# Kernel tuning notes

Hardware: AMD Instinct MI355X
Metric: run time of the kernel (lower is better)

Reference implementation:

```python
import jax, jax.numpy as jnp
import numpy as np

B, S, D = 2, 2048, 1024
N_QK, N_V, N_KNOW = 4096, 4096, 8192
N_HEADS = 16
MAX_K_QK, MAX_K_V, MAX_K_KNOW = 32, 32, 64
LN_EPS = 1e-6


def _unit_norm(key, shape, scale=1.0):
    x = jax.random.normal(key, shape, jnp.float32)
    return x / (jnp.linalg.norm(x, axis=-1, keepdims=True) + 1e-8) * scale


def setup_inputs() -> dict:
    key = jax.random.key(0)
    ks = jax.random.split(key, 12)
    return {
        "x": jax.random.normal(ks[0], (B, S, D), jnp.float32),
        "qk_emb": _unit_norm(ks[1], (N_QK, D)),
        "qk_w": _unit_norm(ks[2], (N_QK, D)),
        "v_emb": _unit_norm(ks[3], (N_V, D)),
        "v_w": _unit_norm(ks[4], (N_V, D)),
        "know_emb": _unit_norm(ks[5], (N_KNOW, D)),
        "know_w": _unit_norm(ks[6], (N_KNOW, D)),
        "tau_attn_k": jax.random.normal(ks[7], (D, 3), jnp.float32) * (1.0 / np.sqrt(D)),
        "tau_attn_b": jnp.zeros((3,), jnp.float32),
        "tau_know_k": jax.random.normal(ks[8], (D, 1), jnp.float32) * (1.0 / np.sqrt(D)),
        "tau_know_b": jnp.zeros((1,), jnp.float32),
        "expand_O": jax.random.normal(ks[9], (D, D), jnp.float32) * 0.02,
        "ln1_scale": jnp.ones((D,), jnp.float32),
        "ln1_bias": jnp.zeros((D,), jnp.float32),
        "ln2_scale": jnp.ones((D,), jnp.float32),
        "ln2_bias": jnp.zeros((D,), jnp.float32),
    }


def _layer_norm(x, scale, bias):
    mean = jnp.mean(x, axis=-1, keepdims=True)
    var = jnp.mean(jnp.square(x - mean), axis=-1, keepdims=True)
    return (x - mean) / jnp.sqrt(var + LN_EPS) * scale + bias


def threshold_gate(scores, tau, max_k):
    # scores: [B,S,N], tau: [B,S,1]
    raw = scores - tau
    gate = jnp.where(raw > 0, raw, 1e-8 * jnp.exp(raw))
    exp_gate = jnp.exp(gate) - 1.0
    topk_vals, _ = jax.lax.top_k(exp_gate, min(max_k, scores.shape[-1]))
    thr = topk_vals[:, :, -1:]
    exp_gate = jnp.where(exp_gate >= thr, exp_gate, 0.0)
    gate_sum = exp_gate.sum(axis=-1, keepdims=True) + 1e-8
    strength = jnp.tanh(exp_gate.max(axis=-1, keepdims=True))
    return exp_gate / gate_sum * strength


@jax.checkpoint
def sense_emit_full(x, emb, w, gate):
    # [B,S,D] @ [D,N] -> gated [B,S,N] -> [B,S,D]
    return ((x @ emb.T) * gate) @ w


def _block(x, qk_emb, qk_w, v_emb, v_w, know_emb, know_w,
           tau_attn_k, tau_attn_b, tau_know_k, tau_know_b,
           expand_O, ln1_scale, ln1_bias, ln2_scale, ln2_bias):
    # ---- attention circuit (deterministic; dropout = identity) ----
    normed = _layer_norm(x, ln1_scale, ln1_bias)
    scores_qk = normed @ qk_emb.T           # [B,S,N_QK]
    scores_v = normed @ v_emb.T             # [B,S,N_V]
    tau_all = normed @ tau_attn_k + tau_attn_b  # [B,S,3]
    g_Q = threshold_gate(scores_qk, tau_all[:, :, 0:1], MAX_K_QK)
    g_K = threshold_gate(scores_qk, tau_all[:, :, 1:2], MAX_K_QK)
    g_V = threshold_gate(scores_v, tau_all[:, :, 2:3], MAX_K_V)
    t_qk = 1.0 / qk_emb.shape[0]
    t_v = 1.0 / v_emb.shape[0]
    a_aux = (((g_Q.mean(axis=(0, 1)) - t_qk) ** 2).sum() * g_Q.shape[-1]
             + ((g_K.mean(axis=(0, 1)) - t_qk) ** 2).sum() * g_K.shape[-1]
             + ((g_V.mean(axis=(0, 1)) - t_v) ** 2).sum() * g_V.shape[-1])

    Q = sense_emit_full(normed, qk_emb, qk_w, g_Q)
    K = sense_emit_full(normed, qk_emb, qk_w, g_K)
    V = sense_emit_full(normed, v_emb, v_w, g_V)

    Bs, Ss, Ds = x.shape
    d_head = Ds // N_HEADS
    Q = Q.reshape(Bs, Ss, N_HEADS, d_head).transpose(0, 2, 1, 3)
    K = K.reshape(Bs, Ss, N_HEADS, d_head).transpose(0, 2, 1, 3)
    V = V.reshape(Bs, Ss, N_HEADS, d_head).transpose(0, 2, 1, 3)
    scale = jnp.sqrt(jnp.float32(d_head))
    attn = jnp.einsum('bhsd,bhtd->bhst', Q, K) / scale
    causal = jnp.tril(jnp.ones((Ss, Ss), dtype=jnp.bool_))
    attn = jnp.where(causal, attn, jnp.finfo(attn.dtype).min)
    attn = jax.nn.softmax(attn, axis=-1)
    out = jnp.einsum('bhst,bhtd->bhsd', attn, V)
    out = out.transpose(0, 2, 1, 3).reshape(Bs, Ss, Ds)
    out = out @ expand_O
    x = x + out

    # ---- knowledge circuit ----
    normed = _layer_norm(x, ln2_scale, ln2_bias)
    scores_k = normed @ know_emb.T          # [B,S,N_KNOW]
    tau_k = normed @ tau_know_k + tau_know_b
    gate = threshold_gate(scores_k, tau_k, MAX_K_KNOW)
    t_k = 1.0 / know_emb.shape[0]
    k_aux = ((gate.mean(axis=(0, 1)) - t_k) ** 2).sum() * know_emb.shape[0]
    know_out = sense_emit_full(normed, know_emb, know_w, gate)
    x = x + know_out
    return x, a_aux + k_aux


def reference(x, qk_emb, qk_w, v_emb, v_w, know_emb, know_w,
              tau_attn_k, tau_attn_b, tau_know_k, tau_know_b,
              expand_O, ln1_scale, ln1_bias, ln2_scale, ln2_bias):
    return _block(x, qk_emb, qk_w, v_emb, v_w, know_emb, know_w,
                  tau_attn_k, tau_attn_b, tau_know_k, tau_know_b,
                  expand_O, ln1_scale, ln1_bias, ln2_scale, ln2_bias)
```

## Files before the change

kernel.cpp:

```cpp
#include <hip/hip_runtime.h>

#define TOK   4096
#define DIM   1024
#define NQK   4096
#define NV    4096
#define NKN   8192
#define SLEN  2048
#define NH    16
#define DH    64
#define CAPA  48
#define CAPK  96
#define APAD  72

typedef float  f32x4  __attribute__((ext_vector_type(4)));
typedef short  short8 __attribute__((ext_vector_type(8)));
typedef unsigned int  u32;
typedef unsigned short u16;

__device__ __forceinline__ u16 f2bf(float f) {
    u32 u = __float_as_uint(f);
    u32 r = (u + 0x7fffu + ((u >> 16) & 1u)) >> 16;
    return (u16)r;
}
__device__ __forceinline__ float bf2f(u16 v) { return __uint_as_float(((u32)v) << 16); }

__device__ __forceinline__ f32x4 mfma_bf16(short8 a, short8 b, f32x4 c) {
    asm volatile("v_mfma_f32_16x16x32_bf16 %0, %1, %2, %0"
                 : "+v"(c) : "v"(a), "v"(b));
    return c;
}

__device__ __forceinline__ void gload16(const u16* g, u16* s) {
    __builtin_amdgcn_global_load_lds((const __attribute__((address_space(1))) void*)g,
                                     (__attribute__((address_space(3))) void*)s, 16, 0, 0);
}

__device__ __forceinline__ float blockReduceF(float v, float* red, int wave, int lane) {
#pragma unroll
    for (int off = 32; off > 0; off >>= 1) v += __shfl_xor(v, off);
    __syncthreads();
    if (lane == 0) red[wave] = v;
    __syncthreads();
    return red[0] + red[1] + red[2] + red[3];
}

__global__ __launch_bounds__(256) void k_f32_to_bf16(const float* __restrict__ in,
                                                     u16* __restrict__ out, int n4) {
    int i = blockIdx.x * 256 + threadIdx.x;
    int stride = gridDim.x * 256;
    for (; i < n4; i += stride) {
        float4 v = reinterpret_cast<const float4*>(in)[i];
        ushort4 o = make_ushort4(f2bf(v.x), f2bf(v.y), f2bf(v.z), f2bf(v.w));
        reinterpret_cast<ushort4*>(out)[i] = o;
    }
}

__global__ __launch_bounds__(256) void k_transpose_bf16(const float* __restrict__ in,
                                                        u16* __restrict__ out) {
    __shared__ float tile[32][33];
    int bx = blockIdx.x * 32;
    int by = blockIdx.y * 32;
    int tx = threadIdx.x & 31;
    int ty = threadIdx.x >> 5;
    for (int r = ty; r < 32; r += 8)
        tile[r][tx] = in[(size_t)(by + r) * DIM + bx + tx];
    __syncthreads();
    for (int r = ty; r < 32; r += 8)
        out[(size_t)(bx + r) * DIM + by + tx] = f2bf(tile[tx][r]);
}

__global__ __launch_bounds__(256) void k_ln_tau(const float* __restrict__ x,
                                                const float* __restrict__ sc,
                                                const float* __restrict__ bi,
                                                const float* __restrict__ tauk,
                                                const float* __restrict__ taub,
                                                int ntau,
                                                u16* __restrict__ nrm,
                                                float* __restrict__ tau_out) {
    __shared__ float red[4];
    int t = blockIdx.x, tid = threadIdx.x, wave = tid >> 6, lane = tid & 63;
    const float4 xv = reinterpret_cast<const float4*>(x + (size_t)t * DIM)[tid];
    float s = xv.x + xv.y + xv.z + xv.w;
    s = blockReduceF(s, red, wave, lane);
    float mean = s * (1.0f / DIM);
    float d0 = xv.x - mean, d1 = xv.y - mean, d2 = xv.z - mean, d3 = xv.w - mean;
    float ss = d0 * d0 + d1 * d1 + d2 * d2 + d3 * d3;
    ss = blockReduceF(ss, red, wave, lane);
    float rstd = rsqrtf(ss * (1.0f / DIM) + 1e-6f);
    const float4 scv = reinterpret_cast<const float4*>(sc)[tid];
    const float4 biv = reinterpret_cast<const float4*>(bi)[tid];
    float n0 = d0 * rstd * scv.x + biv.x;
    float n1 = d1 * rstd * scv.y + biv.y;
    float n2 = d2 * rstd * scv.z + biv.z;
    float n3 = d3 * rstd * scv.w + biv.w;
    ushort4 o = make_ushort4(f2bf(n0), f2bf(n1), f2bf(n2), f2bf(n3));
    reinterpret_cast<ushort4*>(nrm + (size_t)t * DIM)[tid] = o;
    int d = tid * 4;
    for (int j = 0; j < ntau; j++) {
        float p = n0 * tauk[(size_t)(d + 0) * ntau + j] + n1 * tauk[(size_t)(d + 1) * ntau + j]
                + n2 * tauk[(size_t)(d + 2) * ntau + j] + n3 * tauk[(size_t)(d + 3) * ntau + j];
        p = blockReduceF(p, red, wave, lane);
        if (tid == 0) tau_out[(size_t)t * ntau + j] = p + taub[j];
    }
}

template<int TAG>
__global__ __launch_bounds__(256) void k_gemm_bt(const u16* __restrict__ A,
                                                 const u16* __restrict__ B,
                                                 float* __restrict__ C,
                                                 int M, int N, int K,
                                                 const float* __restrict__ res) {
    __shared__ __align__(16) u16 As[4096];
    __shared__ __align__(16) u16 Bs[4096];
    int tid = threadIdx.x;
    int wave = tid >> 6, lane = tid & 63;
    int m0 = blockIdx.y * 128, n0 = blockIdx.x * 128;
    int wm = (wave >> 1) * 64, wn = (wave & 1) * 64;
    int kg = lane >> 4, l15 = lane & 15;

    const u16* gA0 = A + (size_t)(m0 + lane) * K + wave * 8;
    const u16* gA1 = A + (size_t)(m0 + 64 + lane) * K + wave * 8;
    const u16* gB0 = B + (size_t)(n0 + lane) * K + wave * 8;
    const u16* gB1 = B + (size_t)(n0 + 64 + lane) * K + wave * 8;
    u16* sA0 = As + wave * 1024;
    u16* sA1 = As + wave * 1024 + 512;
    u16* sB0 = Bs + wave * 1024;
    u16* sB1 = Bs + wave * 1024 + 512;

    f32x4 acc[4][4];
#pragma unroll
    for (int i = 0; i < 4; i++)
#pragma unroll
        for (int j = 0; j < 4; j++) { f32x4 z = {0.f, 0.f, 0.f, 0.f}; acc[i][j] = z; }

    for (int k0 = 0; k0 < K; k0 += 32) {
        __syncthreads();
        gload16(gA0 + k0, sA0);
        gload16(gA1 + k0, sA1);
        gload16(gB0 + k0, sB0);
        gload16(gB1 + k0, sB1);
        __syncthreads();
        short8 af[4], bg[4];
#pragma unroll
        for (int mi = 0; mi < 4; mi++) {
            int row = wm + mi * 16 + l15;
            af[mi] = *reinterpret_cast<const short8*>(&As[(kg * 128 + row) * 8]);
        }
#pragma unroll
        for (int ni = 0; ni < 4; ni++) {
            int row = wn + ni * 16 + l15;
            bg[ni] = *reinterpret_cast<const short8*>(&Bs[(kg * 128 + row) * 8]);
        }
#pragma unroll
        for (int mi = 0; mi < 4; mi++)
#pragma unroll
            for (int ni = 0; ni < 4; ni++)
                acc[mi][ni] = mfma_bf16(af[mi], bg[ni], acc[mi][ni]);
    }
    asm volatile("s_nop 7\n\ts_nop 7");
#pragma unroll
    for (int mi = 0; mi < 4; mi++) {
#pragma unroll
        for (int ni = 0; ni < 4; ni++) {
            int col = n0 + wn + ni * 16 + l15;
#pragma unroll
            for (int r = 0; r < 4; r++) {
                int rowm = m0 + wm + mi * 16 + (lane >> 4) * 4 + r;
                size_t idx = (size_t)rowm * N + col;
                float v = acc[mi][ni][r];
                if (res) v += res[idx];
                C[idx] = v;
            }
        }
    }
}

__global__ __launch_bounds__(256) void k_gate(const float* __restrict__ scores, int NC, int ksel,
                                              int row_off,
                                              const float* __restrict__ tau, int tau_stride, int tcol0,
                                              int two,
                                              int* __restrict__ sel,
                                              float* __restrict__ vA, float* __restrict__ vB,
                                              int* __restrict__ cnt,
                                              float* __restrict__ csA, float* __restrict__ csB,
                                              int cap) {
    extern __shared__ u32 keys[];
    __shared__ int   hist[256];
    __shared__ int   scnt;
    __shared__ int   dsel;
    __shared__ int   knext;
    __shared__ int   sidx[CAPK];
    __shared__ float sraw[CAPK];
    int r = blockIdx.x, tid = threadIdx.x, wave = tid >> 6, lane = tid & 63;
    int t = row_off + r;

    const float4* srow4 = reinterpret_cast<const float4*>(scores + (size_t)r * NC);
    for (int c = tid; c < NC / 4; c += 256) {
        float4 v = srow4[c];
        u32 u0 = __float_as_uint(v.x), u1 = __float_as_uint(v.y);
        u32 u2 = __float_as_uint(v.z), u3 = __float_as_uint(v.w);
        u0 = (u0 & 0x80000000u) ? ~u0 : (u0 | 0x80000000u);
        u1 = (u1 & 0x80000000u) ? ~u1 : (u1 | 0x80000000u);
        u2 = (u2 & 0x80000000u) ? ~u2 : (u2 | 0x80000000u);
        u3 = (u3 & 0x80000000u) ? ~u3 : (u3 | 0x80000000u);
        reinterpret_cast<uint4*>(keys)[c] = make_uint4(u0, u1, u2, u3);
    }
    if (tid == 0) scnt = 0;

    u32 prefix = 0;
    int krem = ksel;
#pragma unroll
    for (int pass = 0; pass < 4; pass++) {
        int shift = 24 - pass * 8;
        hist[tid] = 0;
        __syncthreads();
        u32 pmask = (pass == 0) ? 0u : (0xFFFFFFFFu << (shift + 8));
        for (int i = tid; i < NC; i += 256) {
            u32 ky = keys[i];
            if ((ky & pmask) == prefix)
                atomicAdd(&hist[(ky >> shift) & 255], 1);
        }
        __syncthreads();
        int v = hist[tid];
#pragma unroll
        for (int off = 1; off < 256; off <<= 1) {
            int other = (tid + off < 256) ? hist[tid + off] : 0;
            __syncthreads();
            v += other;
            hist[tid] = v;
            __syncthreads();
        }
        int sfx = v;
        int sfx_next = (tid < 255) ? hist[tid + 1] : 0;
        if (sfx >= krem && (tid == 255 || sfx_next < krem)) {
            dsel = tid;
            knext = krem - sfx_next;
        }
        __syncthreads();
        prefix |= ((u32)dsel) << shift;
        krem = knext;
        __syncthreads();
    }
    u32 thr = prefix;

    for (int i = tid; i < NC; i += 256) {
        u32 ky = keys[i];
        if (ky >= thr) {
            int p = atomicAdd(&scnt, 1);
            if (p < cap) {
                sidx[p] = i;
                u32 uo = (ky & 0x80000000u) ? (ky & 0x7fffffffu) : ~ky;
                sraw[p] = __uint_as_float(uo);
            }
        }
    }
    __syncthreads();
    int n = scnt < cap ? scnt : cap;
    if (tid == 0) cnt[t] = n;
    if (wave != 0) return;

    float tA = tau[(size_t)t * tau_stride + tcol0];
    float tB = two ? tau[(size_t)t * tau_stride + tcol0 + 1] : 0.f;
    float sumA = 0.f, mxA = -1e30f, sumB = 0.f, mxB = -1e30f;
    for (int i = lane; i < n; i += 64) {
        float sv = sraw[i];
        float rA = sv - tA;
        float gA = rA > 0.f ? rA : 1e-8f * expf(rA);
        float eA = expf(gA) - 1.0f;
        sumA += eA; mxA = fmaxf(mxA, eA);
        if (two) {
            float rB = sv - tB;
            float gB = rB > 0.f ? rB : 1e-8f * expf(rB);
            float eB = expf(gB) - 1.0f;
            sumB += eB; mxB = fmaxf(mxB, eB);
        }
    }
#pragma unroll
    for (int off = 32; off > 0; off >>= 1) {
        sumA += __shfl_xor(sumA, off); mxA = fmaxf(mxA, __shfl_xor(mxA, off));
        sumB += __shfl_xor(sumB, off); mxB = fmaxf(mxB, __shfl_xor(mxB, off));
    }
    float fA = tanhf(mxA) / (sumA + 1e-8f);
    float fB = tanhf(mxB) / (sumB + 1e-8f);
    for (int i = lane; i < n; i += 64) {
        float sv = sraw[i]; int ci = sidx[i];
        float rA = sv - tA;
        float gA = rA > 0.f ? rA : 1e-8f * expf(rA);
        float ga = (expf(gA) - 1.0f) * fA;
        sel[(size_t)t * cap + i] = ci;
        vA[(size_t)t * cap + i] = ga * sv;
        atomicAdd(&csA[ci], ga);
        if (two) {
            float rB = sv - tB;
            float gB = rB > 0.f ? rB : 1e-8f * expf(rB);
            float gb = (expf(gB) - 1.0f) * fB;
            vB[(size_t)t * cap + i] = gb * sv;
            atomicAdd(&csB[ci], gb);
        }
    }
}

__global__ __launch_bounds__(256) void k_gather2(const u16* __restrict__ w,
                                                 const int* __restrict__ sel,
                                                 const float* __restrict__ vA,
                                                 const float* __restrict__ vB,
                                                 const int* __restrict__ cnt, int cap,
                                                 u16* __restrict__ OA, u16* __restrict__ OB) {
    __shared__ int   sI[CAPK];
    __shared__ float sA[CAPK];
    __shared__ float sB[CAPK];
    int t = blockIdx.x, tid = threadIdx.x;
    int n = cnt[t];
    if (tid < n) { sI[tid] = sel[(size_t)t * cap + tid]; sA[tid] = vA[(size_t)t * cap + tid]; sB[tid] = vB[(size_t)t * cap + tid]; }
    __syncthreads();
    float a0 = 0, a1 = 0, a2 = 0, a3 = 0, b0 = 0, b1 = 0, b2 = 0, b3 = 0;
    for (int s = 0; s < n; s++) {
        const ushort4 wv = reinterpret_cast<const ushort4*>(w + (size_t)sI[s] * DIM)[tid];
        float w0 = bf2f(wv.x), w1 = bf2f(wv.y), w2 = bf2f(wv.z), w3 = bf2f(wv.w);
        float va = sA[s], vb = sB[s];
        a0 += va * w0; a1 += va * w1; a2 += va * w2; a3 += va * w3;
        b0 += vb * w0; b1 += vb * w1; b2 += vb * w2; b3 += vb * w3;
    }
    reinterpret_cast<ushort4*>(OA + (size_t)t * DIM)[tid] = make_ushort4(f2bf(a0), f2bf(a1), f2bf(a2), f2bf(a3));
    reinterpret_cast<ushort4*>(OB + (size_t)t * DIM)[tid] = make_ushort4(f2bf(b0), f2bf(b1), f2bf(b2), f2bf(b3));
}

__global__ __launch_bounds__(256) void k_gather1(const u16* __restrict__ w,
                                                 const int* __restrict__ sel,
                                                 const float* __restrict__ vv,
                                                 const int* __restrict__ cnt, int cap,
                                                 u16* __restrict__ O) {
    __shared__ int   sI[CAPK];
    __shared__ float sV[CAPK];
    int t = blockIdx.x, tid = threadIdx.x;
    int n = cnt[t];
    if (tid < n) { sI[tid] = sel[(size_t)t * cap + tid]; sV[tid] = vv[(size_t)t * cap + tid]; }
    __syncthreads();
    float a0 = 0, a1 = 0, a2 = 0, a3 = 0;
    for (int s = 0; s < n; s++) {
        const ushort4 wv = reinterpret_cast<const ushort4*>(w + (size_t)sI[s] * DIM)[tid];
        float va = sV[s];
        a0 += va * bf2f(wv.x); a1 += va * bf2f(wv.y); a2 += va * bf2f(wv.z); a3 += va * bf2f(wv.w);
    }
    reinterpret_cast<ushort4*>(O + (size_t)t * DIM)[tid] = make_ushort4(f2bf(a0), f2bf(a1), f2bf(a2), f2bf(a3));
}

__global__ __launch_bounds__(256) void k_gather_final(const u16* __restrict__ w,
                                                      const int* __restrict__ sel,
                                                      const float* __restrict__ vv,
                                                      const int* __restrict__ cnt, int cap,
                                                      float* __restrict__ io) {
    __shared__ int   sI[CAPK];
    __shared__ float sV[CAPK];
    int t = blockIdx.x, tid = threadIdx.x;
    int n = cnt[t];
    if (tid < n) { sI[tid] = sel[(size_t)t * cap + tid]; sV[tid] = vv[(size_t)t * cap + tid]; }
    __syncthreads();
    float4 base = reinterpret_cast<const float4*>(io + (size_t)t * DIM)[tid];
    float a0 = base.x, a1 = base.y, a2 = base.z, a3 = base.w;
    for (int s = 0; s < n; s++) {
        const ushort4 wv = reinterpret_cast<const ushort4*>(w + (size_t)sI[s] * DIM)[tid];
        float va = sV[s];
        a0 += va * bf2f(wv.x); a1 += va * bf2f(wv.y); a2 += va * bf2f(wv.z); a3 += va * bf2f(wv.w);
    }
    reinterpret_cast<float4*>(io + (size_t)t * DIM)[tid] = make_float4(a0, a1, a2, a3);
}

__global__ __launch_bounds__(256) void k_attn(const u16* __restrict__ Q,
                                              const u16* __restrict__ K,
                                              const u16* __restrict__ V,
                                              u16* __restrict__ O) {
    __shared__ __align__(16) u16 Qs[64 * APAD];
    __shared__ __align__(16) u16 Ks[64 * APAD];
    __shared__ __align__(16) u16 Vt[64 * APAD];
    __shared__ __align__(16) u16 Ps[4][16 * APAD];
    int tid = threadIdx.x, wave = tid >> 6, lane = tid & 63;
    int h = blockIdx.x, bb = blockIdx.y, qt = blockIdx.z;
    int q0 = qt * 64;
    size_t base = ((size_t)bb * SLEN) * DIM + (size_t)h * DH;
    int sr = tid >> 2, sc = (tid & 3) * 16;
    int g = lane >> 4, l15 = lane & 15;

    {
        const u16* qp = Q + base + (size_t)(q0 + sr) * DIM + sc;
        *reinterpret_cast<short8*>(&Qs[sr * APAD + sc])     = *reinterpret_cast<const short8*>(qp);
        *reinterpret_cast<short8*>(&Qs[sr * APAD + sc + 8]) = *reinterpret_cast<const short8*>(qp + 8);
    }
    __syncthreads();
    short8 qa0 = *reinterpret_cast<const short8*>(&Qs[(wave * 16 + l15) * APAD + g * 8]);
    short8 qa1 = *reinterpret_cast<const short8*>(&Qs[(wave * 16 + l15) * APAD + 32 + g * 8]);

    float m[4], l[4];
    f32x4 oacc[4];
#pragma unroll
    for (int i = 0; i < 4; i++) {
        m[i] = -1e30f; l[i] = 0.f;
        f32x4 z = {0.f, 0.f, 0.f, 0.f}; oacc[i] = z;
    }
    u16* pw = &Ps[wave][0];

    for (int kc = 0; kc <= qt; kc++) {
        __syncthreads();
        {
            const u16* kp = K + base + (size_t)(kc * 64 + sr) * DIM + sc;
            *reinterpret_cast<short8*>(&Ks[sr * APAD + sc])     = *reinterpret_cast<const short8*>(kp);
            *reinterpret_cast<short8*>(&Ks[sr * APAD + sc + 8]) = *reinterpret_cast<const short8*>(kp + 8);
            const u16* vp = V + base + (size_t)(kc * 64 + sr) * DIM + sc;
            short8 w0 = *reinterpret_cast<const short8*>(vp);
            short8 w1 = *reinterpret_cast<const short8*>(vp + 8);
            const u16* w0p = reinterpret_cast<const u16*>(&w0);
            const u16* w1p = reinterpret_cast<const u16*>(&w1);
#pragma unroll
            for (int j = 0; j < 16; j++) {
                int d = sc + j;
                int phys = (((sr >> 3) + d + (d >> 4)) & 7);
                Vt[d * APAD + phys * 8 + (sr & 7)] = (j < 8) ? w0p[j] : w1p[j - 8];
            }
        }
        __syncthreads();

        f32x4 s4[4];
#pragma unroll
        for (int ks = 0; ks < 4; ks++) {
            f32x4 z = {0.f, 0.f, 0.f, 0.f}; s4[ks] = z;
            short8 kb0 = *reinterpret_cast<const short8*>(&Ks[(ks * 16 + l15) * APAD + g * 8]);
            short8 kb1 = *reinterpret_cast<const short8*>(&Ks[(ks * 16 + l15) * APAD + 32 + g * 8]);
            s4[ks] = mfma_bf16(qa0, kb0, s4[ks]);
            s4[ks] = mfma_bf16(qa1, kb1, s4[ks]);
        }
        asm volatile("s_nop 7\n\ts_nop 7");

        int key_base = kc * 64 + l15;
#pragma unroll
        for (int ks = 0; ks < 4; ks++) {
            int key = key_base + ks * 16;
#pragma unroll
            for (int r = 0; r < 4; r++) {
                int q_abs = q0 + wave * 16 + g * 4 + r;
                float sv = s4[ks][r] * 0.125f;
                s4[ks][r] = (key > q_abs) ? -1e30f : sv;
            }
        }

#pragma unroll
        for (int r = 0; r < 4; r++) {
            float mx = fmaxf(fmaxf(s4[0][r], s4[1][r]), fmaxf(s4[2][r], s4[3][r]));
            mx = fmaxf(mx, __shfl_xor(mx, 1));
            mx = fmaxf(mx, __shfl_xor(mx, 2));
            mx = fmaxf(mx, __shfl_xor(mx, 4));
            mx = fmaxf(mx, __shfl_xor(mx, 8));
            float mnew = fmaxf(m[r], mx);
            float al = __expf(m[r] - mnew);
            m[r] = mnew;
            float p0 = __expf(s4[0][r] - mnew);
            float p1 = __expf(s4[1][r] - mnew);
            float p2 = __expf(s4[2][r] - mnew);
            float p3 = __expf(s4[3][r] - mnew);
            float ps = p0 + p1 + p2 + p3;
            ps += __shfl_xor(ps, 1);
            ps += __shfl_xor(ps, 2);
            ps += __shfl_xor(ps, 4);
            ps += __shfl_xor(ps, 8);
            l[r] = l[r] * al + ps;
#pragma unroll
            for (int ds_ = 0; ds_ < 4; ds_++) oacc[ds_][r] *= al;
            int row = g * 4 + r;
            pw[row * APAD +  0 + l15] = f2bf(p0);
            pw[row * APAD + 16 + l15] = f2bf(p1);
            pw[row * APAD + 32 + l15] = f2bf(p2);
            pw[row * APAD + 48 + l15] = f2bf(p3);
        }

        short8 pa0 = *reinterpret_cast<const short8*>(&pw[l15 * APAD + g * 8]);
        short8 pa1 = *reinterpret_cast<const short8*>(&pw[l15 * APAD + 32 + g * 8]);
#pragma unroll
        for (int dsub = 0; dsub < 4; dsub++) {
            int d = dsub * 16 + l15;
            int rot = d + (d >> 4);
            short8 vb0 = *reinterpret_cast<const short8*>(&Vt[d * APAD + (((0 + g) + rot) & 7) * 8]);
            short8 vb1 = *reinterpret_cast<const short8*>(&Vt[d * APAD + (((4 + g) + rot) & 7) * 8]);
            oacc[dsub] = mfma_bf16(pa0, vb0, oacc[dsub]);
            oacc[dsub] = mfma_bf16(pa1, vb1, oacc[dsub]);
        }
    }
    asm volatile("s_nop 7\n\ts_nop 7");

#pragma unroll
    for (int r = 0; r < 4; r++) {
        float inv = 1.0f / l[r];
        int row = q0 + wave * 16 + g * 4 + r;
#pragma unroll
        for (int dsub = 0; dsub < 4; dsub++) {
            O[base + (size_t)row * DIM + dsub * 16 + l15] = f2bf(oacc[dsub][r] * inv);
        }
    }
}

__global__ __launch_bounds__(256) void k_aux(const float* __restrict__ cs,
                                             float* __restrict__ out_aux) {
    __shared__ float red[4];
    int gtid = blockIdx.x * 256 + threadIdx.x;
    float acc = 0.f;
    for (int i = gtid; i < 3 * 4096 + 8192; i += gridDim.x * 256) {
        float mean = cs[i] * (1.0f / 4096.0f);
        float tN, Nf;
        if (i < 12288) { tN = 1.0f / 4096.0f; Nf = 4096.0f; }
        else           { tN = 1.0f / 8192.0f; Nf = 8192.0f; }
        float d = mean - tN;
        acc += d * d * Nf;
    }
    acc = blockReduceF(acc, red, threadIdx.x >> 6, threadIdx.x & 63);
    if (threadIdx.x == 0) atomicAdd(out_aux, acc);
}

extern "C" void kernel_launch(void* const* d_in, const int* in_sizes, int n_in,
                              void* d_out, int out_size, void* d_ws, size_t ws_size,
                              hipStream_t stream) {
    const float* x         = (const float*)d_in[0];
    const float* qk_emb    = (const float*)d_in[1];
    const float* qk_w      = (const float*)d_in[2];
    const float* v_emb     = (const float*)d_in[3];
    const float* v_w       = (const float*)d_in[4];
    const float* know_emb  = (const float*)d_in[5];
    const float* know_w    = (const float*)d_in[6];
    const float* tau_attn_k = (const float*)d_in[7];
    const float* tau_attn_b = (const float*)d_in[8];
    const float* tau_know_k = (const float*)d_in[9];
    const float* tau_know_b = (const float*)d_in[10];
    const float* expand_O  = (const float*)d_in[11];
    const float* ln1_s     = (const float*)d_in[12];
    const float* ln1_b     = (const float*)d_in[13];
    const float* ln2_s     = (const float*)d_in[14];
    const float* ln2_b     = (const float*)d_in[15];
    float* out = (float*)d_out;
    char*  ws  = (char*)d_ws;

    u16*   nrm_bf   = (u16*)(ws + 0);
    u16*   qkemb_bf = (u16*)(ws + 8388608);
    u16*   vemb_bf  = (u16*)(ws + 16777216);
    u16*   knemb_bf = (u16*)(ws + 25165824);
    u16*   expT_bf  = (u16*)(ws + 41943040);
    u16*   attn_bf  = (u16*)(ws + 44040192);
    u16*   qkw_bf   = (u16*)(ws + 52428800);
    u16*   vw_bf    = (u16*)(ws + 60817408);
    u16*   knw_bf   = (u16*)(ws + 69206016);
    u16*   Qb       = (u16*)(ws + 85983232);
    u16*   Kb       = (u16*)(ws + 94371840);
    u16*   Vb       = (u16*)(ws + 102760448);
    float* scores   = (float*)(ws + 111149056);
    int*   selQK    = (int*)(ws + 178257920);
    float* valQ     = (float*)(ws + 179044352);
    float* valK     = (float*)(ws + 179830784);
    int*   selV     = (int*)(ws + 180617216);
    float* valV     = (float*)(ws + 181403648);
    int*   selKn    = (int*)(ws + 182190080);
    float* valKn    = (float*)(ws + 183762944);
    int*   cntQK    = (int*)(ws + 185335808);
    int*   cntV     = (int*)(ws + 185352192);
    int*   cntKn    = (int*)(ws + 185368576);
    float* tauA     = (float*)(ws + 185384960);
    float* tauKn    = (float*)(ws + 185434112);
    float* colsum   = (float*)(ws + 185450496);
    const size_t WS_NEEDED = 185532416;
    if (ws_size < WS_NEEDED) return;

    float* colQ = colsum, *colK = colsum + 4096, *colV = colsum + 8192, *colKn = colsum + 12288;

    hipMemsetAsync(colsum, 0, 20480 * sizeof(float), stream);
    hipMemsetAsync(out + (size_t)TOK * DIM, 0, sizeof(float), stream);

    k_f32_to_bf16<<<1024, 256, 0, stream>>>(qk_emb,  qkemb_bf, NQK * DIM / 4);
    k_f32_to_bf16<<<1024, 256, 0, stream>>>(v_emb,   vemb_bf,  NV * DIM / 4);
    k_f32_to_bf16<<<2048, 256, 0, stream>>>(know_emb, knemb_bf, NKN * DIM / 4);
    k_f32_to_bf16<<<1024, 256, 0, stream>>>(qk_w,   qkw_bf, NQK * DIM / 4);
    k_f32_to_bf16<<<1024, 256, 0, stream>>>(v_w,    vw_bf,  NV * DIM / 4);
    k_f32_to_bf16<<<2048, 256, 0, stream>>>(know_w, knw_bf, NKN * DIM / 4);
    k_transpose_bf16<<<dim3(32, 32), 256, 0, stream>>>(expand_O, expT_bf);

    k_ln_tau<<<TOK, 256, 0, stream>>>(x, ln1_s, ln1_b, tau_attn_k, tau_attn_b, 3, nrm_bf, tauA);

    k_gemm_bt<0><<<dim3(NQK / 128, TOK / 128), 256, 0, stream>>>(nrm_bf, qkemb_bf, scores, TOK, NQK, DIM, nullptr);
    k_gate<<<TOK, 256, NQK * sizeof(u32), stream>>>(scores, NQK, 32, 0, tauA, 3, 0, 1,
                                                    selQK, valQ, valK, cntQK, colQ, colK, CAPA);
    k_gemm_bt<1><<<dim3(NV / 128, TOK / 128), 256, 0, stream>>>(nrm_bf, vemb_bf, scores, TOK, NV, DIM, nullptr);
    k_gate<<<TOK, 256, NV * sizeof(u32), stream>>>(scores, NV, 32, 0, tauA, 3, 2, 0,
                                                   selV, valV, nullptr, cntV, colV, nullptr, CAPA);

    k_gather2<<<TOK, 256, 0, stream>>>(qkw_bf, selQK, valQ, valK, cntQK, CAPA, Qb, Kb);
    k_gather1<<<TOK, 256, 0, stream>>>(vw_bf, selV, valV, cntV, CAPA, Vb);

    k_attn<<<dim3(NH, 2, SLEN / 64), 256, 0, stream>>>(Qb, Kb, Vb, attn_bf);

    k_gemm_bt<2><<<dim3(DIM / 128, TOK / 128), 256, 0, stream>>>(attn_bf, expT_bf, out, TOK, DIM, DIM, x);

    k_ln_tau<<<TOK, 256, 0, stream>>>(out, ln2_s, ln2_b, tau_know_k, tau_know_b, 1, nrm_bf, tauKn);

    for (int c = 0; c < 2; c++) {
        k_gemm_bt<3><<<dim3(NKN / 128, 2048 / 128), 256, 0, stream>>>(
            nrm_bf + (size_t)c * 2048 * DIM, knemb_bf, scores, 2048, NKN, DIM, nullptr);
        k_gate<<<2048, 256, NKN * sizeof(u32), stream>>>(scores, NKN, 64, c * 2048, tauKn, 1, 0, 0,
                                                         selKn, valKn, nullptr, cntKn, colKn, nullptr, CAPK);
    }

    k_gather_final<<<TOK, 256, 0, stream>>>(knw_bf, selKn, valKn, cntKn, CAPK, out);

    k_aux<<<20, 256, 0, stream>>>(colsum, out + (size_t)TOK * DIM);
}
```

Baseline: 842.8 us.

## Emit bf16 sortable score keys from GEMM epilogue and shorten radix select

The score GEMMs now write 16-bit order-preserving bf16 keys instead of fp32 scores, which halves score-buffer traffic and removes the key conversion step in the gate kernel. The radix select drops from four passes to two, and shared memory per gate block shrinks. The six weight conversion launches are merged into one kernel, and the attention grid is reordered to launch heavy causal tiles first. Ranking scores at bf16 precision can change ties and the top-k selection compared with fp32.

```diff
diff --git a/kernel.cpp b/kernel.cpp
--- a/kernel.cpp
+++ b/kernel.cpp
@@ -24,6 +24,13 @@
 }
 __device__ __forceinline__ float bf2f(u16 v) { return __uint_as_float(((u32)v) << 16); }
 
+__device__ __forceinline__ u16 bfkey(u16 b) {
+    return (b & 0x8000u) ? (u16)(~b) : (u16)(b | 0x8000u);
+}
+__device__ __forceinline__ u16 keybf(u16 k) {
+    return (k & 0x8000u) ? (u16)(k & 0x7fffu) : (u16)(~k);
+}
+
 __device__ __forceinline__ f32x4 mfma_bf16(short8 a, short8 b, f32x4 c) {
     asm volatile("v_mfma_f32_16x16x32_bf16 %0, %1, %2, %0"
                  : "+v"(c) : "v"(a), "v"(b));
@@ -44,14 +51,26 @@
     return red[0] + red[1] + red[2] + red[3];
 }
 
-__global__ __launch_bounds__(256) void k_f32_to_bf16(const float* __restrict__ in,
-                                                     u16* __restrict__ out, int n4) {
-    int i = blockIdx.x * 256 + threadIdx.x;
-    int stride = gridDim.x * 256;
-    for (; i < n4; i += stride) {
-        float4 v = reinterpret_cast<const float4*>(in)[i];
-        ushort4 o = make_ushort4(f2bf(v.x), f2bf(v.y), f2bf(v.z), f2bf(v.w));
-        reinterpret_cast<ushort4*>(out)[i] = o;
+__global__ __launch_bounds__(256) void k_convert_all(const float* __restrict__ p0,
+                                                     const float* __restrict__ p1,
+                                                     const float* __restrict__ p2,
+                                                     const float* __restrict__ p3,
+                                                     const float* __restrict__ p4,
+                                                     const float* __restrict__ p5,
+                                                     u16* __restrict__ o0, u16* __restrict__ o1,
+                                                     u16* __restrict__ o2, u16* __restrict__ o3,
+                                                     u16* __restrict__ o4, u16* __restrict__ o5) {
+    const int S0 = 1048576, S1 = 2097152, S2 = 4194304, S3 = 5242880, S4 = 6291456, S5 = 8388608;
+    for (int i = blockIdx.x * 256 + threadIdx.x; i < S5; i += gridDim.x * 256) {
+        const float* in; u16* out; int off;
+        if (i < S0)      { in = p0; out = o0; off = i; }
+        else if (i < S1) { in = p1; out = o1; off = i - S0; }
+        else if (i < S2) { in = p2; out = o2; off = i - S1; }
+        else if (i < S3) { in = p3; out = o3; off = i - S2; }
+        else if (i < S4) { in = p4; out = o4; off = i - S3; }
+        else             { in = p5; out = o5; off = i - S4; }
+        float4 v = reinterpret_cast<const float4*>(in)[off];
+        reinterpret_cast<ushort4*>(out)[off] = make_ushort4(f2bf(v.x), f2bf(v.y), f2bf(v.z), f2bf(v.w));
     }
 }
 
@@ -104,10 +123,10 @@
     }
 }
 
-template<int TAG>
+template<int TAG, int KEYOUT>
 __global__ __launch_bounds__(256) void k_gemm_bt(const u16* __restrict__ A,
                                                  const u16* __restrict__ B,
-                                                 float* __restrict__ C,
+                                                 void* __restrict__ Cv,
                                                  int M, int N, int K,
                                                  const float* __restrict__ res) {
     __shared__ __align__(16) u16 As[4096];
@@ -168,14 +187,18 @@
                 int rowm = m0 + wm + mi * 16 + (lane >> 4) * 4 + r;
                 size_t idx = (size_t)rowm * N + col;
                 float v = acc[mi][ni][r];
-                if (res) v += res[idx];
-                C[idx] = v;
+                if (KEYOUT) {
+                    ((u16*)Cv)[idx] = bfkey(f2bf(v));
+                } else {
+                    if (res) v += res[idx];
+                    ((float*)Cv)[idx] = v;
+                }
             }
         }
     }
 }
 
-__global__ __launch_bounds__(256) void k_gate(const float* __restrict__ scores, int NC, int ksel,
+__global__ __launch_bounds__(256) void k_gate(const u16* __restrict__ keys_g, int NC, int ksel,
                                               int row_off,
                                               const float* __restrict__ tau, int tau_stride, int tcol0,
                                               int two,
@@ -184,7 +207,7 @@
                                               int* __restrict__ cnt,
                                               float* __restrict__ csA, float* __restrict__ csB,
                                               int cap) {
-    extern __shared__ u32 keys[];
+    extern __shared__ u16 keys[];
     __shared__ int   hist[256];
     __shared__ int   scnt;
     __shared__ int   dsel;
@@ -194,27 +217,19 @@
     int r = blockIdx.x, tid = threadIdx.x, wave = tid >> 6, lane = tid & 63;
     int t = row_off + r;
 
-    const float4* srow4 = reinterpret_cast<const float4*>(scores + (size_t)r * NC);
-    for (int c = tid; c < NC / 4; c += 256) {
-        float4 v = srow4[c];
-        u32 u0 = __float_as_uint(v.x), u1 = __float_as_uint(v.y);
-        u32 u2 = __float_as_uint(v.z), u3 = __float_as_uint(v.w);
-        u0 = (u0 & 0x80000000u) ? ~u0 : (u0 | 0x80000000u);
-        u1 = (u1 & 0x80000000u) ? ~u1 : (u1 | 0x80000000u);
-        u2 = (u2 & 0x80000000u) ? ~u2 : (u2 | 0x80000000u);
-        u3 = (u3 & 0x80000000u) ? ~u3 : (u3 | 0x80000000u);
-        reinterpret_cast<uint4*>(keys)[c] = make_uint4(u0, u1, u2, u3);
-    }
+    const uint4* srow8 = reinterpret_cast<const uint4*>(keys_g + (size_t)r * NC);
+    for (int c = tid; c < NC / 8; c += 256)
+        reinterpret_cast<uint4*>(keys)[c] = srow8[c];
     if (tid == 0) scnt = 0;
 
     u32 prefix = 0;
     int krem = ksel;
 #pragma unroll
-    for (int pass = 0; pass < 4; pass++) {
-        int shift = 24 - pass * 8;
+    for (int pass = 0; pass < 2; pass++) {
+        int shift = 8 - pass * 8;
         hist[tid] = 0;
         __syncthreads();
-        u32 pmask = (pass == 0) ? 0u : (0xFFFFFFFFu << (shift + 8));
+        u32 pmask = (pass == 0) ? 0u : 0xFF00u;
         for (int i = tid; i < NC; i += 256) {
             u32 ky = keys[i];
             if ((ky & pmask) == prefix)
@@ -249,8 +264,7 @@
             int p = atomicAdd(&scnt, 1);
             if (p < cap) {
                 sidx[p] = i;
-                u32 uo = (ky & 0x80000000u) ? (ky & 0x7fffffffu) : ~ky;
-                sraw[p] = __uint_as_float(uo);
+                sraw[p] = bf2f(keybf((u16)ky));
             }
         }
     }
@@ -375,7 +389,8 @@
     __shared__ __align__(16) u16 Vt[64 * APAD];
     __shared__ __align__(16) u16 Ps[4][16 * APAD];
     int tid = threadIdx.x, wave = tid >> 6, lane = tid & 63;
-    int h = blockIdx.x, bb = blockIdx.y, qt = blockIdx.z;
+    int qt = gridDim.x - 1 - blockIdx.x;
+    int h = blockIdx.y, bb = blockIdx.z;
     int q0 = qt * 64;
     size_t base = ((size_t)bb * SLEN) * DIM + (size_t)h * DH;
     int sr = tid >> 2, sc = (tid & 3) * 16;
@@ -547,7 +562,7 @@
     u16*   Qb       = (u16*)(ws + 85983232);
     u16*   Kb       = (u16*)(ws + 94371840);
     u16*   Vb       = (u16*)(ws + 102760448);
-    float* scores   = (float*)(ws + 111149056);
+    u16*   keysbuf  = (u16*)(ws + 111149056);
     int*   selQK    = (int*)(ws + 178257920);
     float* valQ     = (float*)(ws + 179044352);
     float* valK     = (float*)(ws + 179830784);
@@ -569,36 +584,32 @@
     hipMemsetAsync(colsum, 0, 20480 * sizeof(float), stream);
     hipMemsetAsync(out + (size_t)TOK * DIM, 0, sizeof(float), stream);
 
-    k_f32_to_bf16<<<1024, 256, 0, stream>>>(qk_emb,  qkemb_bf, NQK * DIM / 4);
-    k_f32_to_bf16<<<1024, 256, 0, stream>>>(v_emb,   vemb_bf,  NV * DIM / 4);
-    k_f32_to_bf16<<<2048, 256, 0, stream>>>(know_emb, knemb_bf, NKN * DIM / 4);
-    k_f32_to_bf16<<<1024, 256, 0, stream>>>(qk_w,   qkw_bf, NQK * DIM / 4);
-    k_f32_to_bf16<<<1024, 256, 0, stream>>>(v_w,    vw_bf,  NV * DIM / 4);
-    k_f32_to_bf16<<<2048, 256, 0, stream>>>(know_w, knw_bf, NKN * DIM / 4);
+    k_convert_all<<<2048, 256, 0, stream>>>(qk_emb, v_emb, know_emb, qk_w, v_w, know_w,
+                                            qkemb_bf, vemb_bf, knemb_bf, qkw_bf, vw_bf, knw_bf);
     k_transpose_bf16<<<dim3(32, 32), 256, 0, stream>>>(expand_O, expT_bf);
 
     k_ln_tau<<<TOK, 256, 0, stream>>>(x, ln1_s, ln1_b, tau_attn_k, tau_attn_b, 3, nrm_bf, tauA);
 
-    k_gemm_bt<0><<<dim3(NQK / 128, TOK / 128), 256, 0, stream>>>(nrm_bf, qkemb_bf, scores, TOK, NQK, DIM, nullptr);
-    k_gate<<<TOK, 256, NQK * sizeof(u32), stream>>>(scores, NQK, 32, 0, tauA, 3, 0, 1,
+    k_gemm_bt<0, 1><<<dim3(NQK / 128, TOK / 128), 256, 0, stream>>>(nrm_bf, qkemb_bf, keysbuf, TOK, NQK, DIM, nullptr);
+    k_gate<<<TOK, 256, NQK * sizeof(u16), stream>>>(keysbuf, NQK, 32, 0, tauA, 3, 0, 1,
                                                     selQK, valQ, valK, cntQK, colQ, colK, CAPA);
-    k_gemm_bt<1><<<dim3(NV / 128, TOK / 128), 256, 0, stream>>>(nrm_bf, vemb_bf, scores, TOK, NV, DIM, nullptr);
-    k_gate<<<TOK, 256, NV * sizeof(u32), stream>>>(scores, NV, 32, 0, tauA, 3, 2, 0,
+    k_gemm_bt<1, 1><<<dim3(NV / 128, TOK / 128), 256, 0, stream>>>(nrm_bf, vemb_bf, keysbuf, TOK, NV, DIM, nullptr);
+    k_gate<<<TOK, 256, NV * sizeof(u16), stream>>>(keysbuf, NV, 32, 0, tauA, 3, 2, 0,
                                                    selV, valV, nullptr, cntV, colV, nullptr, CAPA);
 
     k_gather2<<<TOK, 256, 0, stream>>>(qkw_bf, selQK, valQ, valK, cntQK, CAPA, Qb, Kb);
     k_gather1<<<TOK, 256, 0, stream>>>(vw_bf, selV, valV, cntV, CAPA, Vb);
 
-    k_attn<<<dim3(NH, 2, SLEN / 64), 256, 0, stream>>>(Qb, Kb, Vb, attn_bf);
-
-    k_gemm_bt<2><<<dim3(DIM / 128, TOK / 128), 256, 0, stream>>>(attn_bf, expT_bf, out, TOK, DIM, DIM, x);
+    k_attn<<<dim3(SLEN / 64, NH, 2), 256, 0, stream>>>(Qb, Kb, Vb, attn_bf);
+
+    k_gemm_bt<2, 0><<<dim3(DIM / 128, TOK / 128), 256, 0, stream>>>(attn_bf, expT_bf, out, TOK, DIM, DIM, x);
 
     k_ln_tau<<<TOK, 256, 0, stream>>>(out, ln2_s, ln2_b, tau_know_k, tau_know_b, 1, nrm_bf, tauKn);
 
     for (int c = 0; c < 2; c++) {
-        k_gemm_bt<3><<<dim3(NKN / 128, 2048 / 128), 256, 0, stream>>>(
-            nrm_bf + (size_t)c * 2048 * DIM, knemb_bf, scores, 2048, NKN, DIM, nullptr);
-        k_gate<<<2048, 256, NKN * sizeof(u32), stream>>>(scores, NKN, 64, c * 2048, tauKn, 1, 0, 0,
+        k_gemm_bt<3, 1><<<dim3(NKN / 128, 2048 / 128), 256, 0, stream>>>(
+            nrm_bf + (size_t)c * 2048 * DIM, knemb_bf, keysbuf, 2048, NKN, DIM, nullptr);
+        k_gate<<<2048, 256, NKN * sizeof(u16), stream>>>(keysbuf, NKN, 64, c * 2048, tauKn, 1, 0, 0,
                                                          selKn, valKn, nullptr, cntKn, colKn, nullptr, CAPK);
     }
 
```

After: 818.6 us. -2.9%, faster.
